# Optimization experiments

Measured on AMD Instinct MI355X. Metric: run time of the kernel, lower is better.

The kernel has to match this reference:

```python
import jax, jax.numpy as jnp
import numpy as np

GRID_H, GRID_W = 32, 32
THRESHOLD = 1.0
SMOOTH = 0.5


def setup_inputs() -> dict:
    key = jax.random.key(0)
    x = jax.random.normal(key, (64, GRID_H * GRID_W, 768), dtype=jnp.float32)
    return {"x": x}


def reference(x) -> jnp.ndarray:
    B, N, D = x.shape
    H, W = GRID_H, GRID_W
    xr = x.reshape(B, H, W, D)

    # L2 norm of neighbor differences (same as torch.norm(diff, dim=-1))
    diff_h = xr[:, :, 1:, :] - xr[:, :, :-1, :]            # [B, H, W-1, D]
    diff_v = xr[:, 1:, :, :] - xr[:, :-1, :, :]            # [B, H-1, W, D]
    anomaly_h = jnp.sqrt(jnp.sum(diff_h * diff_h, axis=-1))  # [B, H, W-1]
    anomaly_v = jnp.sqrt(jnp.sum(diff_v * diff_v, axis=-1))  # [B, H-1, W]

    # Torch code uses .any() over the batch dim: a patch is anomalous for ALL
    # batch elements if ANY batch element exceeds the threshold.
    exceed_h = jnp.any(anomaly_h > THRESHOLD, axis=0)      # [H, W-1]
    exceed_v = jnp.any(anomaly_v > THRESHOLD, axis=0)      # [H-1, W]

    # Interior patches: i in [1, H-2], j in [1, W-2].
    # Conditions checked per (i, j): ah[i, j-1], ah[i, j], av[i-1, j], av[i, j]
    mask = (exceed_h[1:H - 1, 0:W - 2]
            | exceed_h[1:H - 1, 1:W - 1]
            | exceed_v[0:H - 2, 1:W - 1]
            | exceed_v[1:H - 1, 1:W - 1])                  # [H-2, W-2]

    # 4-neighbor average (all reads from the ORIGINAL xr, as in the torch code)
    avg = (xr[:, 0:H - 2, 1:W - 1, :] + xr[:, 2:H, 1:W - 1, :]
           + xr[:, 1:H - 1, 0:W - 2, :] + xr[:, 1:H - 1, 2:W, :]) * 0.25

    center = xr[:, 1:H - 1, 1:W - 1, :]
    blended = (1.0 - SMOOTH) * center + SMOOTH * avg
    interior = jnp.where(mask[None, :, :, None], blended, center)

    out = xr.at[:, 1:H - 1, 1:W - 1, :].set(interior)
    return out.reshape(B, N, D)
```

## Files before the change

kernel.cpp:

```cpp
#include <hip/hip_runtime.h>

#define THRESH 1.0f

__global__ __launch_bounds__(192) void edge_flags_kernel(
    const float* __restrict__ x, int* __restrict__ flags) {
  __shared__ float red[3];
  __shared__ int sdone;
  const int e = blockIdx.x;
  const int t = threadIdx.x;
  if (t == 0) sdone = 0;
  __syncthreads();

  int p0, p1;
  if (e < 992) {
    int i = e / 31; int j = e - i * 31;
    p0 = i * 32 + j; p1 = p0 + 1;
  } else {
    int e2 = e - 992; int i = e2 >> 5; int j = e2 & 31;
    p0 = i * 32 + j; p1 = p0 + 32;
  }

  const int lane = t & 63;
  const int wid  = t >> 6;

  for (int b = 0; b < 64; ++b) {
    const float4* A = (const float4*)(x + ((size_t)b * 1024 + p0) * 768);
    const float4* B = (const float4*)(x + ((size_t)b * 1024 + p1) * 768);
    float4 va = A[t];
    float4 vb = B[t];
    float dx = va.x - vb.x, dy = va.y - vb.y;
    float dz = va.z - vb.z, dw = va.w - vb.w;
    float s = dx * dx + dy * dy + dz * dz + dw * dw;
#pragma unroll
    for (int off = 32; off > 0; off >>= 1) s += __shfl_down(s, off, 64);
    if (lane == 0) red[wid] = s;
    __syncthreads();
    if (t == 0) {
      float tot = red[0] + red[1] + red[2];
      if (tot > THRESH) sdone = 1;
    }
    __syncthreads();
    if (sdone) break;
  }
  if (t == 0) flags[e] = sdone;
}

__global__ __launch_bounds__(192) void apply_kernel(
    const float* __restrict__ x, const int* __restrict__ flags,
    float* __restrict__ out) {
  const int p    = blockIdx.x;
  const int xcd  = p & 7;
  const int slot = p >> 3;
  const int b    = (xcd << 3) | (slot >> 10);
  const int n    = slot & 1023;
  const int i    = n >> 5, j = n & 31;
  const int t    = threadIdx.x;
  const size_t base = ((size_t)b * 1024 + n) * 192 + t;
  const float4* xv = (const float4*)x;
  float4* ov = (float4*)out;

  int m = 0;
  if (i >= 1 && i <= 30 && j >= 1 && j <= 30) {
    const int* fh = flags;
    const int* fv = flags + 992;
    m = fh[i * 31 + (j - 1)] | fh[i * 31 + j] |
        fv[(i - 1) * 32 + j] | fv[i * 32 + j];
  }

  float4 c = xv[base];
  if (m) {
    float4 l = xv[base - 192];
    float4 r = xv[base + 192];
    float4 u = xv[base - 32 * 192];
    float4 d = xv[base + 32 * 192];
    float4 res;
    res.x = 0.5f * c.x + 0.125f * ((l.x + r.x) + (u.x + d.x));
    res.y = 0.5f * c.y + 0.125f * ((l.y + r.y) + (u.y + d.y));
    res.z = 0.5f * c.z + 0.125f * ((l.z + r.z) + (u.z + d.z));
    res.w = 0.5f * c.w + 0.125f * ((l.w + r.w) + (u.w + d.w));
    ov[base] = res;
  } else {
    ov[base] = c;
  }
}

extern "C" void kernel_launch(void* const* d_in, const int* in_sizes, int n_in,
                              void* d_out, int out_size, void* d_ws,
                              size_t ws_size, hipStream_t stream) {
  const float* x = (const float*)d_in[0];
  float* out = (float*)d_out;
  int* flags = (int*)d_ws;

  edge_flags_kernel<<<1984, 192, 0, stream>>>(x, flags);
  apply_kernel<<<64 * 1024, 192, 0, stream>>>(x, flags, out);
}
```

Baseline: 344.3 us.

## Process a full grid row per block in apply kernel with LDS masks and nontemporal stores

The apply kernel now gives each block a whole image row of 32 patches with 256 threads looping 24 times, instead of one block per patch. The per-patch masks for the row are computed once into shared memory, and outputs go out with nontemporal stores. Ext-vector float4 math replaces the per-component code. This cuts block launch and flag-load overhead and keeps streaming writes from polluting the cache, but the grid shrinks to 2048 blocks, which may lower memory-level parallelism.

Measured after the change: 367.4 us. 1.07x slower.

```diff
diff --git a/kernel.cpp b/kernel.cpp
--- a/kernel.cpp
+++ b/kernel.cpp
@@ -1,6 +1,8 @@
 #include <hip/hip_runtime.h>
 
 #define THRESH 1.0f
+
+typedef float f4 __attribute__((ext_vector_type(4)));
 
 __global__ __launch_bounds__(192) void edge_flags_kernel(
     const float* __restrict__ x, int* __restrict__ flags) {
@@ -24,13 +26,10 @@
   const int wid  = t >> 6;
 
   for (int b = 0; b < 64; ++b) {
-    const float4* A = (const float4*)(x + ((size_t)b * 1024 + p0) * 768);
-    const float4* B = (const float4*)(x + ((size_t)b * 1024 + p1) * 768);
-    float4 va = A[t];
-    float4 vb = B[t];
-    float dx = va.x - vb.x, dy = va.y - vb.y;
-    float dz = va.z - vb.z, dw = va.w - vb.w;
-    float s = dx * dx + dy * dy + dz * dz + dw * dw;
+    const f4* A = (const f4*)(x + ((size_t)b * 1024 + p0) * 768);
+    const f4* B = (const f4*)(x + ((size_t)b * 1024 + p1) * 768);
+    f4 d = A[t] - B[t];
+    float s = d.x * d.x + d.y * d.y + d.z * d.z + d.w * d.w;
 #pragma unroll
     for (int off = 32; off > 0; off >>= 1) s += __shfl_down(s, off, 64);
     if (lane == 0) red[wid] = s;
@@ -45,42 +44,49 @@
   if (t == 0) flags[e] = sdone;
 }
 
-__global__ __launch_bounds__(192) void apply_kernel(
+__global__ __launch_bounds__(256) void apply_kernel(
     const float* __restrict__ x, const int* __restrict__ flags,
     float* __restrict__ out) {
+  __shared__ int mask_lds[32];
   const int p    = blockIdx.x;
   const int xcd  = p & 7;
   const int slot = p >> 3;
-  const int b    = (xcd << 3) | (slot >> 10);
-  const int n    = slot & 1023;
-  const int i    = n >> 5, j = n & 31;
+  const int b    = (xcd << 3) | (slot >> 5);
+  const int i    = slot & 31;
   const int t    = threadIdx.x;
-  const size_t base = ((size_t)b * 1024 + n) * 192 + t;
-  const float4* xv = (const float4*)x;
-  float4* ov = (float4*)out;
 
-  int m = 0;
-  if (i >= 1 && i <= 30 && j >= 1 && j <= 30) {
-    const int* fh = flags;
-    const int* fv = flags + 992;
-    m = fh[i * 31 + (j - 1)] | fh[i * 31 + j] |
-        fv[(i - 1) * 32 + j] | fv[i * 32 + j];
+  if (t < 32) {
+    int j = t, m = 0;
+    if (i >= 1 && i <= 30 && j >= 1 && j <= 30) {
+      const int* fh = flags;
+      const int* fv = flags + 992;
+      m = fh[i * 31 + (j - 1)] | fh[i * 31 + j] |
+          fv[(i - 1) * 32 + j] | fv[i * 32 + j];
+    }
+    mask_lds[j] = m;
   }
+  __syncthreads();
 
-  float4 c = xv[base];
-  if (m) {
-    float4 l = xv[base - 192];
-    float4 r = xv[base + 192];
-    float4 u = xv[base - 32 * 192];
-    float4 d = xv[base + 32 * 192];
-    float4 res;
-    res.x = 0.5f * c.x + 0.125f * ((l.x + r.x) + (u.x + d.x));
-    res.y = 0.5f * c.y + 0.125f * ((l.y + r.y) + (u.y + d.y));
-    res.z = 0.5f * c.z + 0.125f * ((l.z + r.z) + (u.z + d.z));
-    res.w = 0.5f * c.w + 0.125f * ((l.w + r.w) + (u.w + d.w));
-    ov[base] = res;
-  } else {
-    ov[base] = c;
+  const f4* xv = (const f4*)x;
+  f4* ov = (f4*)out;
+  const size_t base = ((size_t)b * 1024 + (size_t)i * 32) * 192;
+
+#pragma unroll 8
+  for (int it = 0; it < 24; ++it) {
+    const int idx = t + it * 256;
+    const int j   = (unsigned)idx / 192u;
+    const size_t e = base + idx;
+    f4 c = xv[e];
+    if (mask_lds[j]) {
+      f4 l = xv[e - 192];
+      f4 r = xv[e + 192];
+      f4 u = xv[e - 6144];
+      f4 d = xv[e + 6144];
+      f4 res = 0.5f * c + 0.125f * ((l + r) + (u + d));
+      __builtin_nontemporal_store(res, &ov[e]);
+    } else {
+      __builtin_nontemporal_store(c, &ov[e]);
+    }
   }
 }
 
@@ -92,5 +98,5 @@
   int* flags = (int*)d_ws;
 
   edge_flags_kernel<<<1984, 192, 0, stream>>>(x, flags);
-  apply_kernel<<<64 * 1024, 192, 0, stream>>>(x, flags, out);
+  apply_kernel<<<64 * 32, 256, 0, stream>>>(x, flags, out);
 }
```
